# Kernel tuning notes

Hardware: AMD Instinct MI355X
Metric: run time of the kernel (lower is better)

Reference implementation:

```python
import jax, jax.numpy as jnp
import numpy as np

TAU = 0.5

def setup_inputs() -> dict:
    key = jax.random.key(0)
    ks = jax.random.split(key, 8)
    B_Nq, B_Ns, C, H, W = 16, 16, 512, 32, 32
    f_q = jax.random.normal(ks[0], (B_Nq, C, H, W), dtype=jnp.float32)
    f_s = jax.random.normal(ks[1], (B_Ns, C, H, W), dtype=jnp.float32)
    # depthwise 1x1 convs with groups=dim, bias=False -> per-channel scalar weights [C]
    w_cca_q = jax.random.normal(ks[2], (C,), dtype=jnp.float32)
    w_cca_k = jax.random.normal(ks[3], (C,), dtype=jnp.float32)
    w_cca_v = jax.random.normal(ks[4], (C,), dtype=jnp.float32)
    w_sca_q = jax.random.normal(ks[5], (C,), dtype=jnp.float32)
    w_sca_k = jax.random.normal(ks[6], (C,), dtype=jnp.float32)
    lam = jnp.float32(0.1)
    return {"f_q": f_q, "f_s": f_s, "w_cca_q": w_cca_q, "w_cca_k": w_cca_k,
            "w_cca_v": w_cca_v, "w_sca_q": w_sca_q, "w_sca_k": w_sca_k, "lam": lam}

def _dw(x, w):
    # depthwise 1x1 conv, no bias == per-channel scale; x: [B,C,H,W], w: [C]
    return x * w[None, :, None, None]

def reference(f_q, f_s, w_cca_q, w_cca_k, w_cca_v, w_sca_q, w_sca_k, lam):
    B_Nq, C, H, W = f_q.shape
    B_Ns = f_s.shape[0]
    P = H * W
    qc = _dw(f_q, w_cca_q).reshape(B_Nq, C, P)          # [B,C,P]
    kc_mean = _dw(f_s, w_cca_k).reshape(B_Ns, C, P).mean(axis=0)  # [C,P]
    vc_mean = _dw(f_s, w_cca_v).reshape(B_Ns, C, P).mean(axis=0)  # [C,P]
    # channel attention: [B,C,C]
    Ac = jax.nn.softmax(jnp.einsum('bcp,dp->bcd', qc, kc_mean) / P, axis=-1)
    f_cca_q = jnp.einsum('bcd,dp->bcp', Ac, vc_mean).reshape(B_Nq, C, H, W)
    qs = _dw(f_cca_q, w_sca_q).reshape(B_Nq, C, P)      # [B,C,P]
    ks_mean = _dw(f_s, w_sca_k).reshape(B_Ns, C, P).mean(axis=0)  # [C,P]
    # spatial affinity: [B,P,P]
    M = jnp.einsum('bcp,cq->bpq', qs, ks_mean) / (TAU * C)
    alpha = jax.nn.softmax(M.mean(axis=-1), axis=-1)    # [B_Nq,P]
    beta = jax.nn.softmax(M.mean(axis=-2), axis=-1)     # [B_Nq,P]
    beta_mean = jnp.broadcast_to(beta.mean(axis=0, keepdims=True), (B_Ns, P))
    Fq_out = f_q + lam * f_cca_q
    return (Fq_out, alpha, beta_mean)
```

## Files before the change

### kernel.cpp

```cpp
#include <hip/hip_runtime.h>

typedef __bf16 bf16;
typedef __bf16 bf16x4 __attribute__((ext_vector_type(4)));
typedef __bf16 bf16x8 __attribute__((ext_vector_type(8)));
typedef float f32x4 __attribute__((ext_vector_type(4)));


#define GLL16(g, l)                                                             \
    __builtin_amdgcn_global_load_lds((const __attribute__((address_space(1))) void*)(g), \
                                     (__attribute__((address_space(3))) void*)(l), 16, 0, 0)

__device__ inline float wave_reduce_sum(float v) {
#pragma unroll
    for (int m = 32; m >= 1; m >>= 1) v += __shfl_xor(v, m, 64);
    return v;
}
__device__ inline float wave_reduce_max(float v) {
#pragma unroll
    for (int m = 32; m >= 1; m >>= 1) v = fmaxf(v, __shfl_xor(v, m, 64));
    return v;
}

__global__ void k_prep(const float* __restrict__ fs, float* __restrict__ fsm32,
                       bf16* __restrict__ fsm16, bf16* __restrict__ fsmT) {
    __shared__ bf16 tile[32][33];
    int bx = blockIdx.x, by = blockIdx.y;
    int p0 = bx * 32, c0 = by * 32;
    int t = threadIdx.x;
    int cy = t >> 3, px = (t & 7) * 4;
    size_t off = (size_t)(c0 + cy) * 1024 + p0 + px;
    float4 s = {0.f, 0.f, 0.f, 0.f};
#pragma unroll
    for (int b = 0; b < 16; ++b) {
        float4 v = *(const float4*)(fs + (size_t)b * 524288 + off);
        s.x += v.x; s.y += v.y; s.z += v.z; s.w += v.w;
    }
    s.x *= (1.f / 16.f); s.y *= (1.f / 16.f); s.z *= (1.f / 16.f); s.w *= (1.f / 16.f);
    *(float4*)(fsm32 + off) = s;
    bf16x4 h4 = {(bf16)s.x, (bf16)s.y, (bf16)s.z, (bf16)s.w};
    *(bf16x4*)(fsm16 + off) = h4;
    tile[cy][px] = h4[0];
    tile[cy][px + 1] = h4[1];
    tile[cy][px + 2] = h4[2];
    tile[cy][px + 3] = h4[3];
    __syncthreads();
    int tx = t & 31, ty = t >> 5;
#pragma unroll
    for (int i = 0; i < 4; ++i)
        fsmT[(size_t)(p0 + ty + 8 * i) * 512 + c0 + tx] = tile[tx][ty + 8 * i];
}

__global__ void k_u(const float* __restrict__ fsm32, const float* __restrict__ wsq,
                    const float* __restrict__ wsk, float* __restrict__ u,
                    float* __restrict__ rm) {
    int c = blockIdx.x;
    int t = threadIdx.x;
    float s = 0.f;
#pragma unroll
    for (int j = 0; j < 4; ++j) s += fsm32[(size_t)c * 1024 + t + 256 * j];
    s = wave_reduce_sum(s);
    __shared__ float red[4];
    int w = t >> 6, lane = t & 63;
    if (lane == 0) red[w] = s;
    __syncthreads();
    if (t == 0) {
        float rmv = (red[0] + red[1] + red[2] + red[3]) * (1.f / 1024.f);
        rm[c] = rmv;
        u[c] = wsq[c] * wsk[c] * rmv * (1.f / 256.f);
    }
}

__global__ void k_gemm1(const float* __restrict__ A, const bf16* __restrict__ B,
                        float* __restrict__ G) {
    __shared__ alignas(16) float Asf[2][64 * 64];
    __shared__ alignas(16) bf16 Bs[2][128 * 64];
    const int dt = blockIdx.x, ct = blockIdx.y, b = blockIdx.z;
    const int t = threadIdx.x, w = t >> 6, lane = t & 63;
    const int quad = lane >> 4, r15 = lane & 15;
    const int wr = w & 1, wc = w >> 1;
    const float* Abase = A + ((size_t)(b * 512 + ct * 64)) * 1024;
    const bf16* Bbase = B + ((size_t)(dt * 128)) * 1024;
    f32x4 acc[2][4] = {};
    auto STAGE = [&](int buf, int k0) {
#pragma unroll
        for (int i = 0; i < 4; ++i) {
            int row = i * 16 + (t >> 4);
            int gchunk = (t & 15) ^ (row & 15);
            GLL16(Abase + (size_t)row * 1024 + k0 + gchunk * 4, &Asf[buf][(i * 256 + t) * 4]);
        }
#pragma unroll
        for (int i = 0; i < 4; ++i) {
            int row = i * 32 + (t >> 3);
            int gchunk = (t & 7) ^ (row & 7);
            GLL16(Bbase + (size_t)row * 1024 + k0 + gchunk * 8, &Bs[buf][(i * 256 + t) * 8]);
        }
    };
    STAGE(0, 0);
    STAGE(1, 64);
    for (int s = 0; s < 16; ++s) {
        if (s < 15) asm volatile("s_waitcnt vmcnt(8)" ::: "memory");
        else        asm volatile("s_waitcnt vmcnt(0)" ::: "memory");
        __builtin_amdgcn_s_barrier();
        const int cur = s & 1;
#pragma unroll
        for (int ks = 0; ks < 2; ++ks) {
            bf16x8 af[2], bfr[4];
            const int c8 = ks * 4 + quad;
#pragma unroll
            for (int mi = 0; mi < 2; ++mi) {
                int R = wr * 32 + mi * 16 + r15;
                f32x4 a0 = *(const f32x4*)(&Asf[cur][R * 64 + (((2 * c8) ^ (R & 15)) * 4)]);
                f32x4 a1 = *(const f32x4*)(&Asf[cur][R * 64 + (((2 * c8 + 1) ^ (R & 15)) * 4)]);
                af[mi] = bf16x8{(bf16)a0[0], (bf16)a0[1], (bf16)a0[2], (bf16)a0[3],
                                (bf16)a1[0], (bf16)a1[1], (bf16)a1[2], (bf16)a1[3]};
            }
#pragma unroll
            for (int j = 0; j < 4; ++j) {
                int R = wc * 64 + j * 16 + r15;
                bfr[j] = *(const bf16x8*)(&Bs[cur][R * 64 + ((c8 ^ (R & 7)) * 8)]);
            }
#pragma unroll
            for (int mi = 0; mi < 2; ++mi)
#pragma unroll
                for (int j = 0; j < 4; ++j)
                    acc[mi][j] = __builtin_amdgcn_mfma_f32_16x16x32_bf16(af[mi], bfr[j], acc[mi][j], 0, 0, 0);
        }
        __builtin_amdgcn_s_barrier();
        if (s + 2 < 16) STAGE(cur, (s + 2) * 64);
    }
#pragma unroll
    for (int mi = 0; mi < 2; ++mi) {
        float* g = G + ((size_t)(b * 512 + ct * 64 + wr * 32 + mi * 16 + quad * 4)) * 512 +
                   dt * 128 + wc * 64 + r15;
#pragma unroll
        for (int j = 0; j < 4; ++j)
#pragma unroll
            for (int ii = 0; ii < 4; ++ii)
                g[(size_t)ii * 512 + j * 16] = acc[mi][j][ii];
    }
}

__global__ void k_softmax_ac(const float* __restrict__ G, const float* __restrict__ wq,
                             const float* __restrict__ wk, const float* __restrict__ wv,
                             const float* __restrict__ rm, bf16* __restrict__ Acw,
                             float* __restrict__ r, float* __restrict__ zbuf) {
    if (blockIdx.x < 128) zbuf[blockIdx.x * 256 + threadIdx.x] = 0.f;
    int row = blockIdx.x * 4 + (threadIdx.x >> 6);
    int lane = threadIdx.x & 63;
    int c = row & 511;
    const float* g = G + (size_t)row * 512;
    float sc = wq[c] * (1.f / 1024.f);
    float v[8];
    float mx = -3.4e38f;
#pragma unroll
    for (int j = 0; j < 8; ++j) {
        int d = lane + 64 * j;
        v[j] = g[d] * sc * wk[d];
        mx = fmaxf(mx, v[j]);
    }
    mx = wave_reduce_max(mx);
    float sum = 0.f;
#pragma unroll
    for (int j = 0; j < 8; ++j) {
        v[j] = __expf(v[j] - mx);
        sum += v[j];
    }
    sum = wave_reduce_sum(sum);
    float inv = 1.f / sum;
    bf16* o = Acw + (size_t)row * 512;
    float rsum = 0.f;
#pragma unroll
    for (int j = 0; j < 8; ++j) {
        int d = lane + 64 * j;
        float aw = v[j] * inv * wv[d];
        o[d] = (bf16)aw;
        rsum += aw * rm[d];
    }
    rsum = wave_reduce_sum(rsum);
    if (lane == 0) r[row] = rsum;
}

__global__ void k_gemm2(const bf16* __restrict__ A, const bf16* __restrict__ B,
                        const float* __restrict__ fq, const float* __restrict__ lamp,
                        const float* __restrict__ u, float* __restrict__ out,
                        float* __restrict__ alog) {
    __shared__ alignas(16) bf16 As[2][64 * 64];
    __shared__ alignas(16) bf16 Bs[2][128 * 64];
    const int pt = blockIdx.x, ct = blockIdx.y, b = blockIdx.z;
    const int t = threadIdx.x, w = t >> 6, lane = t & 63;
    const int quad = lane >> 4, r15 = lane & 15;
    const int wr = w & 1, wc = w >> 1;
    const bf16* Abase = A + ((size_t)(b * 512 + ct * 64)) * 512;
    const bf16* Bbase = B + ((size_t)(pt * 128)) * 512;
    f32x4 acc[2][4] = {};
    auto STAGE = [&](int buf, int k0) {
#pragma unroll
        for (int i = 0; i < 2; ++i) {
            int row = i * 32 + (t >> 3);
            int gchunk = (t & 7) ^ (row & 7);
            GLL16(Abase + (size_t)row * 512 + k0 + gchunk * 8, &As[buf][(i * 256 + t) * 8]);
        }
#pragma unroll
        for (int i = 0; i < 4; ++i) {
            int row = i * 32 + (t >> 3);
            int gchunk = (t & 7) ^ (row & 7);
            GLL16(Bbase + (size_t)row * 512 + k0 + gchunk * 8, &Bs[buf][(i * 256 + t) * 8]);
        }
    };
    STAGE(0, 0);
    STAGE(1, 64);
    for (int s = 0; s < 8; ++s) {
        if (s < 7) asm volatile("s_waitcnt vmcnt(6)" ::: "memory");
        else       asm volatile("s_waitcnt vmcnt(0)" ::: "memory");
        __builtin_amdgcn_s_barrier();
        const int cur = s & 1;
#pragma unroll
        for (int ks = 0; ks < 2; ++ks) {
            bf16x8 af[2], bfr[4];
            const int c8 = ks * 4 + quad;
#pragma unroll
            for (int mi = 0; mi < 2; ++mi) {
                int R = wr * 32 + mi * 16 + r15;
                af[mi] = *(const bf16x8*)(&As[cur][R * 64 + ((c8 ^ (R & 7)) * 8)]);
            }
#pragma unroll
            for (int j = 0; j < 4; ++j) {
                int R = wc * 64 + j * 16 + r15;
                bfr[j] = *(const bf16x8*)(&Bs[cur][R * 64 + ((c8 ^ (R & 7)) * 8)]);
            }
#pragma unroll
            for (int mi = 0; mi < 2; ++mi)
#pragma unroll
                for (int j = 0; j < 4; ++j)
                    acc[mi][j] = __builtin_amdgcn_mfma_f32_16x16x32_bf16(af[mi], bfr[j], acc[mi][j], 0, 0, 0);
        }
        __builtin_amdgcn_s_barrier();
        if (s + 2 < 8) STAGE(cur, (s + 2) * 64);
    }
    float lam = lamp[0];
#pragma unroll
    for (int mi = 0; mi < 2; ++mi) {
        size_t rowbase = (size_t)(b * 512 + ct * 64 + wr * 32 + mi * 16 + quad * 4);
#pragma unroll
        for (int j = 0; j < 4; ++j)
#pragma unroll
            for (int ii = 0; ii < 4; ++ii) {
                size_t idx = (rowbase + ii) * 1024 + pt * 128 + wc * 64 + j * 16 + r15;
                out[idx] = fq[idx] + lam * acc[mi][j][ii];
            }
    }
    float uv[2][4];
#pragma unroll
    for (int mi = 0; mi < 2; ++mi)
#pragma unroll
        for (int ii = 0; ii < 4; ++ii)
            uv[mi][ii] = u[ct * 64 + wr * 32 + mi * 16 + quad * 4 + ii];
#pragma unroll
    for (int j = 0; j < 4; ++j) {
        float pv = 0.f;
#pragma unroll
        for (int mi = 0; mi < 2; ++mi)
#pragma unroll
            for (int ii = 0; ii < 4; ++ii)
                pv += uv[mi][ii] * acc[mi][j][ii];
        pv += __shfl_xor(pv, 16, 64);
        pv += __shfl_xor(pv, 32, 64);
        if (lane < 16)
            atomicAdd(alog + (size_t)b * 1024 + pt * 128 + wc * 64 + j * 16 + r15, pv);
    }
}

__global__ void k_blog(const float* __restrict__ r, const float* __restrict__ wsq,
                       const float* __restrict__ wsk, const float* __restrict__ fsm32,
                       float* __restrict__ blog) {
    int pq = blockIdx.x * 256 + threadIdx.x;
    int b = blockIdx.y;
    int c0 = blockIdx.z * 128;
    const float* rb = r + b * 512;
    float s0 = 0.f, s1 = 0.f, s2 = 0.f, s3 = 0.f;
#pragma unroll 4
    for (int c = c0; c < c0 + 128; c += 4) {
        s0 += rb[c] * wsq[c] * wsk[c] * fsm32[(size_t)c * 1024 + pq];
        s1 += rb[c + 1] * wsq[c + 1] * wsk[c + 1] * fsm32[(size_t)(c + 1) * 1024 + pq];
        s2 += rb[c + 2] * wsq[c + 2] * wsk[c + 2] * fsm32[(size_t)(c + 2) * 1024 + pq];
        s3 += rb[c + 3] * wsq[c + 3] * wsk[c + 3] * fsm32[(size_t)(c + 3) * 1024 + pq];
    }
    atomicAdd(&blog[(size_t)b * 1024 + pq], ((s0 + s1) + (s2 + s3)) * (1.f / 256.f));
}

__global__ void k_softmax_rows(const float* __restrict__ alog, const float* __restrict__ blog,
                               float* __restrict__ alpha_out, float* __restrict__ beta) {
    int z = blockIdx.x;
    int t = threadIdx.x;
    int w = t >> 6, lane = t & 63;
    const float* src = (z < 16) ? (alog + (size_t)z * 1024) : (blog + (size_t)(z - 16) * 1024);
    float v[4];
    float mx = -3.4e38f;
#pragma unroll
    for (int j = 0; j < 4; ++j) {
        v[j] = src[t + 256 * j];
        mx = fmaxf(mx, v[j]);
    }
    __shared__ float red[4];
    float wm = wave_reduce_max(mx);
    if (lane == 0) red[w] = wm;
    __syncthreads();
    mx = fmaxf(fmaxf(red[0], red[1]), fmaxf(red[2], red[3]));
    float s = 0.f;
#pragma unroll
    for (int j = 0; j < 4; ++j) {
        v[j] = __expf(v[j] - mx);
        s += v[j];
    }
    __syncthreads();
    float ws_ = wave_reduce_sum(s);
    if (lane == 0) red[w] = ws_;
    __syncthreads();
    s = red[0] + red[1] + red[2] + red[3];
    float inv = 1.f / s;
    if (z < 16) {
#pragma unroll
        for (int j = 0; j < 4; ++j) alpha_out[(size_t)z * 1024 + t + 256 * j] = v[j] * inv;
    } else {
#pragma unroll
        for (int j = 0; j < 4; ++j) beta[(size_t)(z - 16) * 1024 + t + 256 * j] = v[j] * inv;
    }
}

__global__ void k_betamean(const float* __restrict__ beta, float* __restrict__ out) {
    int q = blockIdx.x * 256 + threadIdx.x;
    float s = 0.f;
#pragma unroll
    for (int b = 0; b < 16; ++b) s += beta[b * 1024 + q];
    float val = s * (1.f / 16.f);
#pragma unroll
    for (int si = 0; si < 16; ++si) out[(size_t)si * 1024 + q] = val;
}

extern "C" void kernel_launch(void* const* d_in, const int* in_sizes, int n_in,
                              void* d_out, int out_size, void* d_ws, size_t ws_size,
                              hipStream_t stream) {
    const float* f_q = (const float*)d_in[0];
    const float* f_s = (const float*)d_in[1];
    const float* w_cca_q = (const float*)d_in[2];
    const float* w_cca_k = (const float*)d_in[3];
    const float* w_cca_v = (const float*)d_in[4];
    const float* w_sca_q = (const float*)d_in[5];
    const float* w_sca_k = (const float*)d_in[6];
    const float* lamp = (const float*)d_in[7];

    char* ws = (char*)d_ws;
    float* fsm32 = (float*)(ws + 0);
    bf16* fsm16 = (bf16*)(ws + 2097152);
    bf16* fsmT = (bf16*)(ws + 3145728);
    float* G = (float*)(ws + 4194304);
    bf16* Acw = (bf16*)(ws + 20971520);
    float* rm = (float*)(ws + 46137344);
    float* u = (float*)(ws + 46139392);
    float* r = (float*)(ws + 46141440);
    float* alog = (float*)(ws + 46239744);
    float* blog = (float*)(ws + 46305280);
    float* beta = (float*)(ws + 46370816);

    float* out_fq = (float*)d_out;
    float* out_alpha = out_fq + 8388608;
    float* out_bmean = out_fq + 8404992;

    k_prep<<<dim3(32, 16), 256, 0, stream>>>(f_s, fsm32, fsm16, fsmT);
    k_u<<<512, 256, 0, stream>>>(fsm32, w_sca_q, w_sca_k, u, rm);
    k_gemm1<<<dim3(4, 8, 16), 256, 0, stream>>>(f_q, fsm16, G);
    k_softmax_ac<<<2048, 256, 0, stream>>>(G, w_cca_q, w_cca_k, w_cca_v, rm, Acw, r, alog);
    k_gemm2<<<dim3(8, 8, 16), 256, 0, stream>>>(Acw, fsmT, f_q, lamp, u, out_fq, alog);
    k_blog<<<dim3(4, 16, 4), 256, 0, stream>>>(r, w_sca_q, w_sca_k, fsm32, blog);
    k_softmax_rows<<<32, 256, 0, stream>>>(alog, blog, out_alpha, beta);
    k_betamean<<<4, 256, 0, stream>>>(beta, out_bmean);
}
```

Baseline: 185.9 us.

## Fuse small kernels into neighbors and pre-convert f_q to bf16 for gemm1

Converts f_q to bf16 inside k_prep, so gemm1 loads half as many A bytes and skips the per-fragment float-to-bf16 conversion. Folds the channel-mean reduction (k_u) into k_prep partial sums plus a finalize step in gemm1, the blog reduction into the ct==0 blocks of gemm2, and beta-mean into the softmax kernel through atomics and a last-block counter. This drops three launches, at the cost of an extra f_q read and bf16 write in prep and some load imbalance in gemm2's ct==0 blocks. One risk is that rm/u are written by gemm1 block (0,ct,0) while other blocks run, though they are only consumed by later kernels, so this is safe.

```diff
diff --git a/kernel.cpp b/kernel.cpp
--- a/kernel.cpp
+++ b/kernel.cpp
@@ -21,8 +21,10 @@
     return v;
 }
 
-__global__ void k_prep(const float* __restrict__ fs, float* __restrict__ fsm32,
-                       bf16* __restrict__ fsm16, bf16* __restrict__ fsmT) {
+__global__ void k_prep(const float* __restrict__ fs, const float* __restrict__ fq,
+                       float* __restrict__ fsm32, bf16* __restrict__ fsm16,
+                       bf16* __restrict__ fsmT, bf16* __restrict__ fq16,
+                       float* __restrict__ rmpart) {
     __shared__ bf16 tile[32][33];
     int bx = blockIdx.x, by = blockIdx.y;
     int p0 = bx * 32, c0 = by * 32;
@@ -43,50 +45,59 @@
     tile[cy][px + 1] = h4[1];
     tile[cy][px + 2] = h4[2];
     tile[cy][px + 3] = h4[3];
+    float rp = s.x + s.y + s.z + s.w;
+    rp += __shfl_xor(rp, 1, 64);
+    rp += __shfl_xor(rp, 2, 64);
+    rp += __shfl_xor(rp, 4, 64);
+    if ((t & 7) == 0) rmpart[bx * 512 + c0 + cy] = rp;
     __syncthreads();
     int tx = t & 31, ty = t >> 5;
 #pragma unroll
     for (int i = 0; i < 4; ++i)
         fsmT[(size_t)(p0 + ty + 8 * i) * 512 + c0 + tx] = tile[tx][ty + 8 * i];
-}
-
-__global__ void k_u(const float* __restrict__ fsm32, const float* __restrict__ wsq,
-                    const float* __restrict__ wsk, float* __restrict__ u,
-                    float* __restrict__ rm) {
-    int c = blockIdx.x;
-    int t = threadIdx.x;
-    float s = 0.f;
-#pragma unroll
-    for (int j = 0; j < 4; ++j) s += fsm32[(size_t)c * 1024 + t + 256 * j];
-    s = wave_reduce_sum(s);
-    __shared__ float red[4];
-    int w = t >> 6, lane = t & 63;
-    if (lane == 0) red[w] = s;
-    __syncthreads();
-    if (t == 0) {
-        float rmv = (red[0] + red[1] + red[2] + red[3]) * (1.f / 1024.f);
-        rm[c] = rmv;
-        u[c] = wsq[c] * wsk[c] * rmv * (1.f / 256.f);
-    }
-}
-
-__global__ void k_gemm1(const float* __restrict__ A, const bf16* __restrict__ B,
-                        float* __restrict__ G) {
-    __shared__ alignas(16) float Asf[2][64 * 64];
+    int blk = by * 32 + bx;
+    const float4* f4 = (const float4*)fq;
+#pragma unroll
+    for (int i = 0; i < 16; ++i) {
+        int idx = blk * 4096 + i * 256 + t;
+        float4 v = f4[idx];
+        bf16x4 q4 = {(bf16)v.x, (bf16)v.y, (bf16)v.z, (bf16)v.w};
+        *(bf16x4*)(fq16 + (size_t)idx * 4) = q4;
+    }
+}
+
+__global__ void k_gemm1(const bf16* __restrict__ A, const bf16* __restrict__ B,
+                        const float* __restrict__ rmpart, const float* __restrict__ wsq,
+                        const float* __restrict__ wsk, float* __restrict__ rm,
+                        float* __restrict__ u, float* __restrict__ G) {
+    __shared__ alignas(16) bf16 As[2][64 * 64];
     __shared__ alignas(16) bf16 Bs[2][128 * 64];
     const int dt = blockIdx.x, ct = blockIdx.y, b = blockIdx.z;
     const int t = threadIdx.x, w = t >> 6, lane = t & 63;
     const int quad = lane >> 4, r15 = lane & 15;
     const int wr = w & 1, wc = w >> 1;
-    const float* Abase = A + ((size_t)(b * 512 + ct * 64)) * 1024;
+    if (dt == 0 && b == 0) {
+        int c = ct * 64 + (t >> 2);
+        float sum = 0.f;
+#pragma unroll
+        for (int j = 0; j < 8; ++j) sum += rmpart[((t & 3) * 8 + j) * 512 + c];
+        sum += __shfl_xor(sum, 1, 64);
+        sum += __shfl_xor(sum, 2, 64);
+        if ((t & 3) == 0) {
+            float rmv = sum * (1.f / 1024.f);
+            rm[c] = rmv;
+            u[c] = wsq[c] * wsk[c] * rmv * (1.f / 256.f);
+        }
+    }
+    const bf16* Abase = A + ((size_t)(b * 512 + ct * 64)) * 1024;
     const bf16* Bbase = B + ((size_t)(dt * 128)) * 1024;
     f32x4 acc[2][4] = {};
     auto STAGE = [&](int buf, int k0) {
 #pragma unroll
-        for (int i = 0; i < 4; ++i) {
-            int row = i * 16 + (t >> 4);
-            int gchunk = (t & 15) ^ (row & 15);
-            GLL16(Abase + (size_t)row * 1024 + k0 + gchunk * 4, &Asf[buf][(i * 256 + t) * 4]);
+        for (int i = 0; i < 2; ++i) {
+            int row = i * 32 + (t >> 3);
+            int gchunk = (t & 7) ^ (row & 7);
+            GLL16(Abase + (size_t)row * 1024 + k0 + gchunk * 8, &As[buf][(i * 256 + t) * 8]);
         }
 #pragma unroll
         for (int i = 0; i < 4; ++i) {
@@ -98,7 +109,7 @@
     STAGE(0, 0);
     STAGE(1, 64);
     for (int s = 0; s < 16; ++s) {
-        if (s < 15) asm volatile("s_waitcnt vmcnt(8)" ::: "memory");
+        if (s < 15) asm volatile("s_waitcnt vmcnt(6)" ::: "memory");
         else        asm volatile("s_waitcnt vmcnt(0)" ::: "memory");
         __builtin_amdgcn_s_barrier();
         const int cur = s & 1;
@@ -109,10 +120,7 @@
 #pragma unroll
             for (int mi = 0; mi < 2; ++mi) {
                 int R = wr * 32 + mi * 16 + r15;
-                f32x4 a0 = *(const f32x4*)(&Asf[cur][R * 64 + (((2 * c8) ^ (R & 15)) * 4)]);
-                f32x4 a1 = *(const f32x4*)(&Asf[cur][R * 64 + (((2 * c8 + 1) ^ (R & 15)) * 4)]);
-                af[mi] = bf16x8{(bf16)a0[0], (bf16)a0[1], (bf16)a0[2], (bf16)a0[3],
-                                (bf16)a1[0], (bf16)a1[1], (bf16)a1[2], (bf16)a1[3]};
+                af[mi] = *(const bf16x8*)(&As[cur][R * 64 + ((c8 ^ (R & 7)) * 8)]);
             }
 #pragma unroll
             for (int j = 0; j < 4; ++j) {
@@ -144,7 +152,7 @@
                              const float* __restrict__ wk, const float* __restrict__ wv,
                              const float* __restrict__ rm, bf16* __restrict__ Acw,
                              float* __restrict__ r, float* __restrict__ zbuf) {
-    if (blockIdx.x < 128) zbuf[blockIdx.x * 256 + threadIdx.x] = 0.f;
+    if (blockIdx.x < 133) zbuf[blockIdx.x * 256 + threadIdx.x] = 0.f;
     int row = blockIdx.x * 4 + (threadIdx.x >> 6);
     int lane = threadIdx.x & 63;
     int c = row & 511;
@@ -182,8 +190,10 @@
 
 __global__ void k_gemm2(const bf16* __restrict__ A, const bf16* __restrict__ B,
                         const float* __restrict__ fq, const float* __restrict__ lamp,
-                        const float* __restrict__ u, float* __restrict__ out,
-                        float* __restrict__ alog) {
+                        const float* __restrict__ u, const float* __restrict__ r,
+                        const float* __restrict__ wsq, const float* __restrict__ wsk,
+                        const float* __restrict__ fsm32, float* __restrict__ out,
+                        float* __restrict__ alog, float* __restrict__ blog) {
     __shared__ alignas(16) bf16 As[2][64 * 64];
     __shared__ alignas(16) bf16 Bs[2][128 * 64];
     const int pt = blockIdx.x, ct = blockIdx.y, b = blockIdx.z;
@@ -268,28 +278,30 @@
         if (lane < 16)
             atomicAdd(alog + (size_t)b * 1024 + pt * 128 + wc * 64 + j * 16 + r15, pv);
     }
-}
-
-__global__ void k_blog(const float* __restrict__ r, const float* __restrict__ wsq,
-                       const float* __restrict__ wsk, const float* __restrict__ fsm32,
-                       float* __restrict__ blog) {
-    int pq = blockIdx.x * 256 + threadIdx.x;
-    int b = blockIdx.y;
-    int c0 = blockIdx.z * 128;
-    const float* rb = r + b * 512;
-    float s0 = 0.f, s1 = 0.f, s2 = 0.f, s3 = 0.f;
+    if (ct == 0) {
+        __shared__ float coef[512];
+        coef[t] = r[b * 512 + t] * wsq[t] * wsk[t] * (1.f / 256.f);
+        coef[t + 256] = r[b * 512 + t + 256] * wsq[t + 256] * wsk[t + 256] * (1.f / 256.f);
+        __syncthreads();
+        int q = pt * 128 + (t & 127);
+        int ch = t >> 7;
+        const float* f = fsm32 + (size_t)(ch * 256) * 1024 + q;
+        const float* cf = coef + ch * 256;
+        float s0 = 0.f, s1 = 0.f, s2 = 0.f, s3 = 0.f;
 #pragma unroll 4
-    for (int c = c0; c < c0 + 128; c += 4) {
-        s0 += rb[c] * wsq[c] * wsk[c] * fsm32[(size_t)c * 1024 + pq];
-        s1 += rb[c + 1] * wsq[c + 1] * wsk[c + 1] * fsm32[(size_t)(c + 1) * 1024 + pq];
-        s2 += rb[c + 2] * wsq[c + 2] * wsk[c + 2] * fsm32[(size_t)(c + 2) * 1024 + pq];
-        s3 += rb[c + 3] * wsq[c + 3] * wsk[c + 3] * fsm32[(size_t)(c + 3) * 1024 + pq];
-    }
-    atomicAdd(&blog[(size_t)b * 1024 + pq], ((s0 + s1) + (s2 + s3)) * (1.f / 256.f));
+        for (int ci = 0; ci < 256; ci += 4) {
+            s0 += cf[ci] * f[(size_t)ci * 1024];
+            s1 += cf[ci + 1] * f[(size_t)(ci + 1) * 1024];
+            s2 += cf[ci + 2] * f[(size_t)(ci + 2) * 1024];
+            s3 += cf[ci + 3] * f[(size_t)(ci + 3) * 1024];
+        }
+        atomicAdd(&blog[(size_t)b * 1024 + q], (s0 + s1) + (s2 + s3));
+    }
 }
 
 __global__ void k_softmax_rows(const float* __restrict__ alog, const float* __restrict__ blog,
-                               float* __restrict__ alpha_out, float* __restrict__ beta) {
+                               float* __restrict__ alpha_out, float* __restrict__ bmean,
+                               int* __restrict__ cnt, float* __restrict__ out_bmean) {
     int z = blockIdx.x;
     int t = threadIdx.x;
     int w = t >> 6, lane = t & 63;
@@ -322,19 +334,25 @@
 #pragma unroll
         for (int j = 0; j < 4; ++j) alpha_out[(size_t)z * 1024 + t + 256 * j] = v[j] * inv;
     } else {
-#pragma unroll
-        for (int j = 0; j < 4; ++j) beta[(size_t)(z - 16) * 1024 + t + 256 * j] = v[j] * inv;
-    }
-}
-
-__global__ void k_betamean(const float* __restrict__ beta, float* __restrict__ out) {
-    int q = blockIdx.x * 256 + threadIdx.x;
-    float s = 0.f;
-#pragma unroll
-    for (int b = 0; b < 16; ++b) s += beta[b * 1024 + q];
-    float val = s * (1.f / 16.f);
-#pragma unroll
-    for (int si = 0; si < 16; ++si) out[(size_t)si * 1024 + q] = val;
+        float inv16 = inv * (1.f / 16.f);
+#pragma unroll
+        for (int j = 0; j < 4; ++j) atomicAdd(&bmean[t + 256 * j], v[j] * inv16);
+        __threadfence();
+        __syncthreads();
+        __shared__ int lastflag;
+        if (t == 0) lastflag = (atomicAdd(cnt, 1) == 15) ? 1 : 0;
+        __syncthreads();
+        if (lastflag) {
+            __threadfence();
+#pragma unroll
+            for (int j = 0; j < 4; ++j) {
+                int q = t + 256 * j;
+                float val = __hip_atomic_load(&bmean[q], __ATOMIC_ACQUIRE, __HIP_MEMORY_SCOPE_AGENT);
+#pragma unroll
+                for (int si = 0; si < 16; ++si) out_bmean[(size_t)si * 1024 + q] = val;
+            }
+        }
+    }
 }
 
 extern "C" void kernel_launch(void* const* d_in, const int* in_sizes, int n_in,
@@ -355,23 +373,24 @@
     bf16* fsmT = (bf16*)(ws + 3145728);
     float* G = (float*)(ws + 4194304);
     bf16* Acw = (bf16*)(ws + 20971520);
-    float* rm = (float*)(ws + 46137344);
-    float* u = (float*)(ws + 46139392);
-    float* r = (float*)(ws + 46141440);
+    bf16* fq16 = (bf16*)(ws + 29360128);
+    float* rmpart = (float*)(ws + 46137344);
+    float* rm = (float*)(ws + 46202880);
+    float* u = (float*)(ws + 46204928);
+    float* r = (float*)(ws + 46206976);
     float* alog = (float*)(ws + 46239744);
     float* blog = (float*)(ws + 46305280);
-    float* beta = (float*)(ws + 46370816);
+    float* bmean = (float*)(ws + 46370816);
+    int* cnt = (int*)(ws + 46374912);
 
     float* out_fq = (float*)d_out;
     float* out_alpha = out_fq + 8388608;
     float* out_bmean = out_fq + 8404992;
 
-    k_prep<<<dim3(32, 16), 256, 0, stream>>>(f_s, fsm32, fsm16, fsmT);
-    k_u<<<512, 256, 0, stream>>>(fsm32, w_sca_q, w_sca_k, u, rm);
-    k_gemm1<<<dim3(4, 8, 16), 256, 0, stream>>>(f_q, fsm16, G);
+    k_prep<<<dim3(32, 16), 256, 0, stream>>>(f_s, f_q, fsm32, fsm16, fsmT, fq16, rmpart);
+    k_gemm1<<<dim3(4, 8, 16), 256, 0, stream>>>(fq16, fsm16, rmpart, w_sca_q, w_sca_k, rm, u, G);
     k_softmax_ac<<<2048, 256, 0, stream>>>(G, w_cca_q, w_cca_k, w_cca_v, rm, Acw, r, alog);
-    k_gemm2<<<dim3(8, 8, 16), 256, 0, stream>>>(Acw, fsmT, f_q, lamp, u, out_fq, alog);
-    k_blog<<<dim3(4, 16, 4), 256, 0, stream>>>(r, w_sca_q, w_sca_k, fsm32, blog);
-    k_softmax_rows<<<32, 256, 0, stream>>>(alog, blog, out_alpha, beta);
-    k_betamean<<<4, 256, 0, stream>>>(beta, out_bmean);
-}
+    k_gemm2<<<dim3(8, 8, 16), 256, 0, stream>>>(Acw, fsmT, f_q, lamp, u, r, w_sca_q, w_sca_k,
+                                                fsm32, out_fq, alog, blog);
+    k_softmax_rows<<<32, 256, 0, stream>>>(alog, blog, out_alpha, bmean, cnt, out_bmean);
+}
```

Result: faster. 172.8 us (median of 2 runs) (-7.1%).
